# Performance work log

Hardware: AMD Instinct MI355X
Metric: run time of the kernel (lower is better)

Reference implementation:

```python
import jax, jax.numpy as jnp
import numpy as np

B, S, D, V = 8, 256, 64, 8192


def setup_inputs() -> dict:
    key = jax.random.key(0)
    k1, k2, k3 = jax.random.split(key, 3)
    x = jax.random.randint(k1, (B, S), 0, V, dtype=jnp.int32)
    # embedding table (nnx.Embed default-ish init scale)
    embed = jax.random.normal(k2, (V, D), dtype=jnp.float32) * 0.02
    # lecun_normal over fan_in = S*D for shape (S, S, D, D)
    fan_in = S * D
    kernel = jax.random.normal(k3, (S, S, D, D), dtype=jnp.float32) * (1.0 / np.sqrt(fan_in))
    return {"x": x, "embed": embed, "kernel": kernel}


def reference(x, embed, kernel):
    # x: [B, S] int tokens -> h: [B, S, D]
    h = embed[x]
    # causal mask over (t, s): output position t attends to source s <= t
    mask = jnp.tril(jnp.ones((S, S), dtype=h.dtype))
    # per-position bilinear token mixing: [B, T, D_out]
    y = jnp.einsum('bsd,tsdo,ts->bto', h, kernel, mask)
    # embed.attend: project back onto vocabulary -> [B, T, V]
    logits = jnp.einsum('bto,vo->btv', y, embed)
    return logits
```

## Files before the change

kernel.cpp:

```cpp
#include <hip/hip_runtime.h>

#define NB 8
#define NS 256
#define ND 64
#define NV 8192
#define CH 16
#define BT_TILE 16
#define NCHUNK 2176

typedef float f32x4 __attribute__((ext_vector_type(4)));

__global__ __launch_bounds__(256) void k_init(const int* __restrict__ x,
                                              const float* __restrict__ embed,
                                              float* __restrict__ h,
                                              float* __restrict__ y) {
    int tid = blockIdx.x * 256 + threadIdx.x;
    int bs = tid >> 6;
    int d  = tid & 63;
    h[tid] = embed[(size_t)x[bs] * ND + d];
    y[tid] = 0.f;
}

__global__ __launch_bounds__(256) void k_transpose(const float* __restrict__ embed,
                                                   float* __restrict__ et) {
    __shared__ float tile[64][65];
    int vbase = blockIdx.x * 64;
    int o = threadIdx.x & 63;
    int r = threadIdx.x >> 6;
    for (int i = r; i < 64; i += 4)
        tile[i][o] = embed[(size_t)(vbase + i) * ND + o];
    __syncthreads();
    for (int i = r; i < 64; i += 4)
        et[(size_t)i * NV + vbase + o] = tile[o][i];
}

__global__ __launch_bounds__(256) void k_bilinear(const float* __restrict__ h,
                                                  const float* __restrict__ K,
                                                  float* __restrict__ y) {
    int L = (NCHUNK - 1) - (int)blockIdx.x;
    int g = 0;
    while (8 * (g + 1) * (g + 2) <= L) g++;
    int rem = L - 8 * g * (g + 1);
    int tq  = rem / (g + 1);
    int t   = 16 * g + tq;
    int c   = rem - tq * (g + 1);
    int s0  = c * CH;
    int ns  = min(t + 1 - s0, CH);

    __shared__ float smem[NB * CH * ND];

    for (int i = threadIdx.x; i < NB * CH * ND; i += 256) {
        int b    = i >> 10;
        int rem2 = i & 1023;
        smem[i] = h[((size_t)b * NS + s0) * ND + rem2];
    }
    __syncthreads();

    int ot = threadIdx.x & 15;
    int dg = threadIdx.x >> 4;
    int o4 = ot * 4;
    int db = dg * 4;

    f32x4 acc[NB];
#pragma unroll
    for (int b = 0; b < NB; b++) acc[b] = (f32x4)(0.f);

    const float* Kt = K + (size_t)t * NS * ND * ND;
    for (int si = 0; si < ns; si++) {
        const float* Ks = Kt + (size_t)(s0 + si) * ND * ND;
#pragma unroll
        for (int i = 0; i < 4; i++) {
            int d = db + i;
            f32x4 k4 = __builtin_nontemporal_load(
                reinterpret_cast<const f32x4*>(Ks + d * ND + o4));
#pragma unroll
            for (int b = 0; b < NB; b++) {
                float hv = smem[b * (CH * ND) + si * ND + d];
                acc[b] += hv * k4;
            }
        }
    }
    __syncthreads();

    f32x4* red = reinterpret_cast<f32x4*>(smem);
#pragma unroll
    for (int b = 0; b < NB; b++) red[(dg * NB + b) * 16 + ot] = acc[b];
    __syncthreads();

    if (threadIdx.x < 128) {
        int b = threadIdx.x >> 4;
        int o = threadIdx.x & 15;
        f32x4 s = (f32x4)(0.f);
#pragma unroll
        for (int gg = 0; gg < 16; gg++)
            s += red[(gg * NB + b) * 16 + o];
        float* yp = y + ((size_t)b * NS + t) * ND + o * 4;
        atomicAdd(yp + 0, s.x);
        atomicAdd(yp + 1, s.y);
        atomicAdd(yp + 2, s.z);
        atomicAdd(yp + 3, s.w);
    }
}

__global__ __launch_bounds__(256) void k_logits(const float* __restrict__ y,
                                                const float* __restrict__ et,
                                                float* __restrict__ out) {
    int bt0 = blockIdx.x * BT_TILE;
    int v4  = blockIdx.y * 1024 + threadIdx.x * 4;

    __shared__ float ylds[BT_TILE][ND];
    for (int i = threadIdx.x; i < BT_TILE * ND; i += 256)
        ylds[i >> 6][i & 63] = y[(size_t)bt0 * ND + i];
    __syncthreads();

    f32x4 acc[BT_TILE];
#pragma unroll
    for (int r = 0; r < BT_TILE; r++) acc[r] = (f32x4)(0.f);

#pragma unroll 4
    for (int o = 0; o < ND; o++) {
        f32x4 e4 = *reinterpret_cast<const f32x4*>(et + (size_t)o * NV + v4);
#pragma unroll
        for (int r = 0; r < BT_TILE; r++) {
            float yv = ylds[r][o];
            acc[r] += yv * e4;
        }
    }

#pragma unroll
    for (int r = 0; r < BT_TILE; r++)
        __builtin_nontemporal_store(acc[r],
            reinterpret_cast<f32x4*>(out + (size_t)(bt0 + r) * NV + v4));
}

extern "C" void kernel_launch(void* const* d_in, const int* in_sizes, int n_in,
                              void* d_out, int out_size, void* d_ws, size_t ws_size,
                              hipStream_t stream) {
    const int*   x     = (const int*)d_in[0];
    const float* embed = (const float*)d_in[1];
    const float* K     = (const float*)d_in[2];
    float* out = (float*)d_out;

    float* h  = (float*)d_ws;
    float* y  = h + NB * NS * ND;
    float* et = y + NB * NS * ND;

    k_init<<<dim3((NB * NS * ND) / 256), 256, 0, stream>>>(x, embed, h, y);
    k_transpose<<<dim3(NV / 64), 256, 0, stream>>>(embed, et);
    k_bilinear<<<dim3(NCHUNK), 256, 0, stream>>>(h, K, y);
    k_logits<<<dim3((NB * NS) / BT_TILE, NV / 1024), 256, 0, stream>>>(y, et, out);
}
```

Measured before the change: 158.6 us.

## Compute vocabulary projection with bf16 MFMA and bf16-cast embedding table

Replaces the fp32 FMA logits kernel with one using 16x16x32 bf16 matrix-core instructions, reading y rows and embedding rows directly as A/B operands. The embedding transpose kernel is replaced by a simple fp32-to-bf16 cast kernel. This aims to cut the ALU cost of the projection, but it lowers input precision to bf16 and stores output as scalars in 64-byte segments rather than 16-byte vectors.

```diff
diff --git a/kernel.cpp b/kernel.cpp
--- a/kernel.cpp
+++ b/kernel.cpp
@@ -5,10 +5,24 @@
 #define ND 64
 #define NV 8192
 #define CH 16
-#define BT_TILE 16
 #define NCHUNK 2176
 
 typedef float f32x4 __attribute__((ext_vector_type(4)));
+typedef short s16x4 __attribute__((ext_vector_type(4)));
+typedef short s16x8 __attribute__((ext_vector_type(8)));
+
+__device__ __forceinline__ short f2bf(float x) {
+    union { float f; unsigned u; } v; v.f = x;
+    unsigned u = v.u + 0x7FFFu + ((v.u >> 16) & 1u);
+    return (short)(u >> 16);
+}
+
+__device__ __forceinline__ s16x8 cvt8(f32x4 lo, f32x4 hi) {
+    s16x8 r;
+    r[0] = f2bf(lo.x); r[1] = f2bf(lo.y); r[2] = f2bf(lo.z); r[3] = f2bf(lo.w);
+    r[4] = f2bf(hi.x); r[5] = f2bf(hi.y); r[6] = f2bf(hi.z); r[7] = f2bf(hi.w);
+    return r;
+}
 
 __global__ __launch_bounds__(256) void k_init(const int* __restrict__ x,
                                               const float* __restrict__ embed,
@@ -21,17 +35,13 @@
     y[tid] = 0.f;
 }
 
-__global__ __launch_bounds__(256) void k_transpose(const float* __restrict__ embed,
-                                                   float* __restrict__ et) {
-    __shared__ float tile[64][65];
-    int vbase = blockIdx.x * 64;
-    int o = threadIdx.x & 63;
-    int r = threadIdx.x >> 6;
-    for (int i = r; i < 64; i += 4)
-        tile[i][o] = embed[(size_t)(vbase + i) * ND + o];
-    __syncthreads();
-    for (int i = r; i < 64; i += 4)
-        et[(size_t)i * NV + vbase + o] = tile[o][i];
+__global__ __launch_bounds__(256) void k_cast(const float* __restrict__ embed,
+                                              short* __restrict__ eb) {
+    int tid = blockIdx.x * 256 + threadIdx.x;
+    f32x4 v = *reinterpret_cast<const f32x4*>(embed + (size_t)tid * 4);
+    s16x4 o;
+    o.x = f2bf(v.x); o.y = f2bf(v.y); o.z = f2bf(v.z); o.w = f2bf(v.w);
+    *reinterpret_cast<s16x4*>(eb + (size_t)tid * 4) = o;
 }
 
 __global__ __launch_bounds__(256) void k_bilinear(const float* __restrict__ h,
@@ -102,35 +112,37 @@
     }
 }
 
-__global__ __launch_bounds__(256) void k_logits(const float* __restrict__ y,
-                                                const float* __restrict__ et,
-                                                float* __restrict__ out) {
-    int bt0 = blockIdx.x * BT_TILE;
-    int v4  = blockIdx.y * 1024 + threadIdx.x * 4;
+__global__ __launch_bounds__(256) void k_logits_mfma(const float* __restrict__ y,
+                                                     const short* __restrict__ eb,
+                                                     float* __restrict__ out) {
+    int bt0  = blockIdx.x * 16;
+    int wave = threadIdx.x >> 6;
+    int lane = threadIdx.x & 63;
+    int m    = lane & 15;
+    int kg   = lane >> 4;
+    int vb0  = blockIdx.y * 1024 + wave * 256;
 
-    __shared__ float ylds[BT_TILE][ND];
-    for (int i = threadIdx.x; i < BT_TILE * ND; i += 256)
-        ylds[i >> 6][i & 63] = y[(size_t)bt0 * ND + i];
-    __syncthreads();
+    const float* yrow = y + (size_t)(bt0 + m) * ND + kg * 8;
+    f32x4 p0 = *reinterpret_cast<const f32x4*>(yrow);
+    f32x4 p1 = *reinterpret_cast<const f32x4*>(yrow + 4);
+    f32x4 p2 = *reinterpret_cast<const f32x4*>(yrow + 32);
+    f32x4 p3 = *reinterpret_cast<const f32x4*>(yrow + 36);
+    s16x8 a0 = cvt8(p0, p1);
+    s16x8 a1 = cvt8(p2, p3);
 
-    f32x4 acc[BT_TILE];
+    for (int nt = 0; nt < 16; nt++) {
+        int v0 = vb0 + nt * 16;
+        const short* erow = eb + (size_t)(v0 + m) * ND + kg * 8;
+        s16x8 b0 = *reinterpret_cast<const s16x8*>(erow);
+        s16x8 b1 = *reinterpret_cast<const s16x8*>(erow + 32);
+        f32x4 cacc = (f32x4)(0.f);
+        cacc = __builtin_amdgcn_mfma_f32_16x16x32_bf16(a0, b0, cacc, 0, 0, 0);
+        cacc = __builtin_amdgcn_mfma_f32_16x16x32_bf16(a1, b1, cacc, 0, 0, 0);
+        float* op = out + (size_t)(bt0 + kg * 4) * NV + v0 + m;
 #pragma unroll
-    for (int r = 0; r < BT_TILE; r++) acc[r] = (f32x4)(0.f);
-
-#pragma unroll 4
-    for (int o = 0; o < ND; o++) {
-        f32x4 e4 = *reinterpret_cast<const f32x4*>(et + (size_t)o * NV + v4);
-#pragma unroll
-        for (int r = 0; r < BT_TILE; r++) {
-            float yv = ylds[r][o];
-            acc[r] += yv * e4;
-        }
+        for (int r = 0; r < 4; r++)
+            __builtin_nontemporal_store(cacc[r], op + (size_t)r * NV);
     }
-
-#pragma unroll
-    for (int r = 0; r < BT_TILE; r++)
-        __builtin_nontemporal_store(acc[r],
-            reinterpret_cast<f32x4*>(out + (size_t)(bt0 + r) * NV + v4));
 }
 
 extern "C" void kernel_launch(void* const* d_in, const int* in_sizes, int n_in,
@@ -143,10 +155,10 @@
 
     float* h  = (float*)d_ws;
     float* y  = h + NB * NS * ND;
-    float* et = y + NB * NS * ND;
+    short* eb = (short*)(y + NB * NS * ND);
 
     k_init<<<dim3((NB * NS * ND) / 256), 256, 0, stream>>>(x, embed, h, y);
-    k_transpose<<<dim3(NV / 64), 256, 0, stream>>>(embed, et);
+    k_cast<<<dim3((NV * ND) / 1024), 256, 0, stream>>>(embed, eb);
     k_bilinear<<<dim3(NCHUNK), 256, 0, stream>>>(h, K, y);
-    k_logits<<<dim3((NB * NS) / BT_TILE, NV / 1024), 256, 0, stream>>>(y, et, out);
+    k_logits_mfma<<<dim3((NB * NS) / 16, NV / 1024), 256, 0, stream>>>(y, eb, out);
 }
```

Result: faster. 149.8 us (-5.6%).
